# Optimization experiments

Hardware: AMD Instinct MI355X
Metric: run time of the kernel (lower is better)

Reference implementation:

```python
import jax, jax.numpy as jnp
import numpy as np

B, S, D, H = 4, 2048, 1024, 16
DK = D // H


def setup_inputs() -> dict:
    key = jax.random.key(0)
    ks = jax.random.split(key, 12)
    s = 1.0 / np.sqrt(D)
    return {
        "query": jax.random.normal(ks[0], (B, S, D), jnp.float32),
        "key": jax.random.normal(ks[1], (B, S, D), jnp.float32),
        "value": jax.random.normal(ks[2], (B, S, D), jnp.float32),
        "attention_mask": jax.random.randint(ks[3], (B, S, S), 0, 2, jnp.int32),
        "w_q": jax.random.uniform(ks[4], (D, D), jnp.float32, -s, s),
        "b_q": jax.random.uniform(ks[5], (D,), jnp.float32, -s, s),
        "w_k": jax.random.uniform(ks[6], (D, D), jnp.float32, -s, s),
        "b_k": jax.random.uniform(ks[7], (D,), jnp.float32, -s, s),
        "w_v": jax.random.uniform(ks[8], (D, D), jnp.float32, -s, s),
        "b_v": jax.random.uniform(ks[9], (D,), jnp.float32, -s, s),
        "w_o": jax.random.uniform(ks[10], (D, D), jnp.float32, -s, s),
        "b_o": jax.random.uniform(ks[11], (D,), jnp.float32, -s, s),
    }


def reference(query, key, value, attention_mask, w_q, b_q, w_k, b_k, w_v, b_v, w_o, b_o):
    # project and split heads: [B,S,D] -> [B,H,S,DK]
    def proj(x, w, b):
        y = jnp.einsum('bsd,ed->bse', x, w) + b  # torch Linear: x @ W.T + b
        return y.reshape(B, S, H, DK).transpose(0, 2, 1, 3)

    q = proj(query, w_q, b_q)
    k = proj(key, w_k, b_k)
    v = proj(value, w_v, b_v)

    scores = jnp.einsum('bhqd,bhkd->bhqk', q, k) / np.sqrt(DK).astype(np.float32)
    mask = attention_mask[:, None, :, :]  # broadcast over heads
    scores = jnp.where(mask == 0, jnp.float32(-1e9), scores)
    attn = jax.nn.softmax(scores, axis=-1)  # dropout is identity in eval
    out = jnp.einsum('bhqk,bhkd->bhqd', attn, v)
    out = out.transpose(0, 2, 1, 3).reshape(B, S, D)
    return jnp.einsum('bsd,ed->bse', out, w_o) + b_o
```

## Files before the change

kernel.cpp:

```cpp
#include <hip/hip_runtime.h>


#define B_ 4
#define S_ 2048
#define D_ 1024
#define H_ 16
#define DK_ 64
#define M_ (B_ * S_)

typedef __attribute__((ext_vector_type(4))) float f32x4;
typedef __attribute__((ext_vector_type(8))) short s16x8;
typedef __attribute__((ext_vector_type(8))) unsigned short u16x8;
typedef __attribute__((ext_vector_type(4))) unsigned short u16x4;

__device__ __forceinline__ unsigned short f2bf(float f) {
    union { float f; unsigned int u; } v; v.f = f;
    unsigned int u = v.u;
    return (unsigned short)((u + 0x7FFFu + ((u >> 16) & 1u)) >> 16);
}

__device__ __forceinline__ void gl2lds16(const unsigned short* g, unsigned short* l) {
    __builtin_amdgcn_global_load_lds((const __attribute__((address_space(1))) void*)g,
                                     (__attribute__((address_space(3))) void*)l, 16, 0, 0);
}

__global__ __launch_bounds__(256) void cvt_bf16(const float* __restrict__ x,
                                                unsigned short* __restrict__ y, int n) {
    int i = (blockIdx.x * 256 + threadIdx.x) * 8;
    if (i + 8 <= n) {
        float4 a = *(const float4*)(x + i);
        float4 b = *(const float4*)(x + i + 4);
        u16x8 r;
        r[0] = f2bf(a.x); r[1] = f2bf(a.y); r[2] = f2bf(a.z); r[3] = f2bf(a.w);
        r[4] = f2bf(b.x); r[5] = f2bf(b.y); r[6] = f2bf(b.z); r[7] = f2bf(b.w);
        *(u16x8*)(y + i) = r;
    }
}

__global__ __launch_bounds__(256) void pack_mask(const int* __restrict__ m,
                                                 unsigned long long* __restrict__ pm) {
    int t = blockIdx.x * 256 + threadIdx.x;
    unsigned long long bits = __ballot(m[t] != 0);
    if ((threadIdx.x & 63) == 0) pm[t >> 6] = bits;
}

template <int MODE>
__global__ __launch_bounds__(256) void gemm_bt(const unsigned short* __restrict__ A,
                                               const unsigned short* __restrict__ Bt,
                                               const float* __restrict__ bias,
                                               float scale, void* __restrict__ Y) {
    __shared__ __align__(16) unsigned short As[128 * 64];
    __shared__ __align__(16) unsigned short Bs[128 * 64];
    const int tid = threadIdx.x;
    const int wave = tid >> 6, lane = tid & 63, quad = lane >> 4, l16 = lane & 15;
    const int m0 = blockIdx.x * 128, n0 = blockIdx.y * 128;
    const int rw = (wave & 1) * 64, cw = (wave >> 1) * 64;
    const int sw = l16 & 7;

    const int srow = tid >> 3, scol = ((tid & 7) ^ (srow & 7)) * 8;
    const unsigned short* ga = A + (size_t)(m0 + srow) * 1024 + scol;
    const unsigned short* gb = Bt + (size_t)(n0 + srow) * 1024 + scol;

    f32x4 acc[4][4];
#pragma unroll
    for (int mi = 0; mi < 4; mi++)
#pragma unroll
        for (int ni = 0; ni < 4; ni++) acc[mi][ni] = (f32x4){0.f, 0.f, 0.f, 0.f};

    for (int k0 = 0; k0 < 1024; k0 += 64) {
#pragma unroll
        for (int r = 0; r < 4; r++) {
            gl2lds16(ga + (size_t)(r * 32) * 1024 + k0, &As[(r * 256 + tid) * 8]);
            gl2lds16(gb + (size_t)(r * 32) * 1024 + k0, &Bs[(r * 256 + tid) * 8]);
        }
        __syncthreads();
#pragma unroll
        for (int kki = 0; kki < 2; kki++) {
            const int xo = ((kki * 4 + quad) ^ sw) * 8;
            s16x8 af[4], bf[4];
#pragma unroll
            for (int mi = 0; mi < 4; mi++)
                af[mi] = *(const s16x8*)&As[(rw + mi * 16 + l16) * 64 + xo];
#pragma unroll
            for (int ni = 0; ni < 4; ni++)
                bf[ni] = *(const s16x8*)&Bs[(cw + ni * 16 + l16) * 64 + xo];
#pragma unroll
            for (int mi = 0; mi < 4; mi++)
#pragma unroll
                for (int ni = 0; ni < 4; ni++)
                    acc[mi][ni] = __builtin_amdgcn_mfma_f32_16x16x32_bf16(af[mi], bf[ni], acc[mi][ni], 0, 0, 0);
        }
        __syncthreads();
    }

    float bv[4];
#pragma unroll
    for (int ni = 0; ni < 4; ni++) bv[ni] = bias[n0 + cw + ni * 16 + l16];
#pragma unroll
    for (int mi = 0; mi < 4; mi++) {
        const int rb = m0 + rw + mi * 16 + quad * 4;
        const int b = rb >> 11, s0 = rb & 2047;
#pragma unroll
        for (int ni = 0; ni < 4; ni++) {
            const int col = n0 + cw + ni * 16 + l16;
            if (MODE == 3) {
#pragma unroll
                for (int i = 0; i < 4; i++)
                    ((float*)Y)[(size_t)(rb + i) * 1024 + col] = (acc[mi][ni][i] + bv[ni]) * scale;
            } else {
                const int h = col >> 6, dk = col & 63;
                if (MODE == 1) {
#pragma unroll
                    for (int i = 0; i < 4; i++)
                        ((unsigned short*)Y)[((size_t)(b * H_ + h) * S_ + s0 + i) * DK_ + dk] =
                            f2bf((acc[mi][ni][i] + bv[ni]) * scale);
                } else {
                    u16x4 pk;
#pragma unroll
                    for (int i = 0; i < 4; i++) pk[i] = f2bf((acc[mi][ni][i] + bv[ni]) * scale);
                    *(u16x4*)&((unsigned short*)Y)[((size_t)(b * H_ + h) * DK_ + dk) * S_ + s0] = pk;
                }
            }
        }
    }
}

__global__ __launch_bounds__(256) void attn_kernel(const unsigned short* __restrict__ Q,
                                                   const unsigned short* __restrict__ K,
                                                   const unsigned short* __restrict__ Vt,
                                                   const unsigned long long* __restrict__ pm,
                                                   unsigned short* __restrict__ ctx) {
    __shared__ __align__(16) unsigned short Ks[64 * 64];
    __shared__ __align__(16) unsigned short Vs[64 * 64];
    __shared__ __align__(16) unsigned short Ps[8 * 16 * 64];

    const int tid = threadIdx.x;
    const int wave = tid >> 6, lane = tid & 63, quad = lane >> 4, l16 = lane & 15;
    const int bh = blockIdx.y, b = bh >> 4, h = bh & 15;
    const int q0 = blockIdx.x * 128;
    const int qbase = q0 + wave * 32;
    const int sw = l16 & 7, q4 = quad * 4, qh = quad >> 1;

    const unsigned short* Kbase = K + (size_t)bh * S_ * DK_;
    const unsigned short* Vbase = Vt + (size_t)bh * DK_ * S_;

    s16x8 qf[2][2];
#pragma unroll
    for (int qb = 0; qb < 2; qb++) {
        const unsigned short* qr = Q + ((size_t)bh * S_ + qbase + qb * 16 + l16) * DK_ + quad * 8;
        qf[qb][0] = *(const s16x8*)qr;
        qf[qb][1] = *(const s16x8*)(qr + 32);
    }
    const unsigned long long* pmq[2];
#pragma unroll
    for (int qb = 0; qb < 2; qb++)
        pmq[qb] = pm + ((size_t)b * S_ + qbase + qb * 16 + l16) * 32;

    s16x8 ones;
#pragma unroll
    for (int j = 0; j < 8; j++) ones[j] = (short)0x3F80;

    f32x4 oacc[2][4], lacc[2];
#pragma unroll
    for (int qb = 0; qb < 2; qb++) {
        lacc[qb] = (f32x4){0.f, 0.f, 0.f, 0.f};
#pragma unroll
        for (int ct = 0; ct < 4; ct++) oacc[qb][ct] = (f32x4){0.f, 0.f, 0.f, 0.f};
    }

    const int sr = tid >> 3, sc = ((tid & 7) ^ (sr & 7)) * 8;

    for (int kt = 0; kt < S_ / 64; kt++) {
        const int k0 = kt * 64;
        gl2lds16(Kbase + (size_t)(k0 + sr) * DK_ + sc, &Ks[tid * 8]);
        gl2lds16(Kbase + (size_t)(k0 + 32 + sr) * DK_ + sc, &Ks[2048 + tid * 8]);
        gl2lds16(Vbase + (size_t)sr * S_ + k0 + sc, &Vs[tid * 8]);
        gl2lds16(Vbase + (size_t)(32 + sr) * S_ + k0 + sc, &Vs[2048 + tid * 8]);
        __syncthreads();

        f32x4 sacc[2][4];
#pragma unroll
        for (int qb = 0; qb < 2; qb++)
#pragma unroll
            for (int ct = 0; ct < 4; ct++) sacc[qb][ct] = (f32x4){0.f, 0.f, 0.f, 0.f};
#pragma unroll
        for (int kki = 0; kki < 2; kki++) {
            const int xo = ((kki * 4 + quad) ^ sw) * 8;
            s16x8 kf[4];
#pragma unroll
            for (int ct = 0; ct < 4; ct++)
                kf[ct] = *(const s16x8*)&Ks[(ct * 16 + l16) * 64 + xo];
#pragma unroll
            for (int qb = 0; qb < 2; qb++)
#pragma unroll
                for (int ct = 0; ct < 4; ct++)
                    sacc[qb][ct] = __builtin_amdgcn_mfma_f32_16x16x32_bf16(kf[ct], qf[qb][kki], sacc[qb][ct], 0, 0, 0);
        }

#pragma unroll
        for (int qb = 0; qb < 2; qb++) {
            unsigned short* pwq = &Ps[(wave * 2 + qb) * 1024];
            const uint2 mv = *(const uint2*)&pmq[qb][kt];
            const unsigned mqx = mv.x >> q4;
            const unsigned mqy = mv.y >> q4;
#pragma unroll
            for (int ct = 0; ct < 4; ct++) {
                const unsigned mq = (ct & 2) ? mqy : mqx;
                unsigned pu[4];
#pragma unroll
                for (int i = 0; i < 4; i++) {
                    const int pos = (ct & 1) * 16 + i;
                    const int mb = __builtin_amdgcn_sbfe(mq, pos, 1);
                    const float p = exp2f(sacc[qb][ct][i]);
                    pu[i] = __float_as_uint(p) & (unsigned)mb;
                }
                const int ch = ((2 * ct + qh) ^ sw) * 8;
#pragma unroll
                for (int t = 0; t < 2; t++) {
                    const unsigned pk = __builtin_amdgcn_perm(pu[2 * t + 1], pu[2 * t], 0x07060302u);
                    *(unsigned*)&pwq[l16 * 64 + ch + ((q4 + 2 * t) & 7)] = pk;
                }
            }
        }

#pragma unroll
        for (int kki = 0; kki < 2; kki++) {
            const int xo = ((kki * 4 + quad) ^ sw) * 8;
            s16x8 vf[4];
#pragma unroll
            for (int ct = 0; ct < 4; ct++)
                vf[ct] = *(const s16x8*)&Vs[(ct * 16 + l16) * 64 + xo];
#pragma unroll
            for (int qb = 0; qb < 2; qb++) {
                s16x8 pf = *(const s16x8*)&Ps[(wave * 2 + qb) * 1024 + l16 * 64 + xo];
#pragma unroll
                for (int ct = 0; ct < 4; ct++)
                    oacc[qb][ct] = __builtin_amdgcn_mfma_f32_16x16x32_bf16(pf, vf[ct], oacc[qb][ct], 0, 0, 0);
                lacc[qb] = __builtin_amdgcn_mfma_f32_16x16x32_bf16(pf, ones, lacc[qb], 0, 0, 0);
            }
        }
        __syncthreads();
    }

#pragma unroll
    for (int qb = 0; qb < 2; qb++) {
        f32x4 rl;
#pragma unroll
        for (int i = 0; i < 4; i++) rl[i] = 1.0f / lacc[qb][i];
#pragma unroll
        for (int ct = 0; ct < 4; ct++) {
            const int col = h * DK_ + ct * 16 + l16;
#pragma unroll
            for (int i = 0; i < 4; i++) {
                const int sg = qbase + qb * 16 + quad * 4 + i;
                ctx[((size_t)(b * S_ + sg)) * D_ + col] = f2bf(oacc[qb][ct][i] * rl[i]);
            }
        }
    }
}

extern "C" void kernel_launch(void* const* d_in, const int* in_sizes, int n_in,
                              void* d_out, int out_size, void* d_ws, size_t ws_size,
                              hipStream_t stream) {
    const float* query = (const float*)d_in[0];
    const float* key   = (const float*)d_in[1];
    const float* value = (const float*)d_in[2];
    const int*   mask  = (const int*)d_in[3];
    const float* w_q = (const float*)d_in[4];
    const float* b_q = (const float*)d_in[5];
    const float* w_k = (const float*)d_in[6];
    const float* b_k = (const float*)d_in[7];
    const float* w_v = (const float*)d_in[8];
    const float* b_v = (const float*)d_in[9];
    const float* w_o = (const float*)d_in[10];
    const float* b_o = (const float*)d_in[11];

    char* ws = (char*)d_ws;
    const size_t XSZ = (size_t)M_ * D_ * 2;
    const size_t WSZ = (size_t)D_ * D_ * 2;
    unsigned short* Xq  = (unsigned short*)(ws);
    unsigned short* Xk  = (unsigned short*)(ws + XSZ);
    unsigned short* Xv  = (unsigned short*)(ws + 2 * XSZ);
    unsigned short* Wq  = (unsigned short*)(ws + 3 * XSZ);
    unsigned short* Wk  = (unsigned short*)(ws + 3 * XSZ + WSZ);
    unsigned short* Wv  = (unsigned short*)(ws + 3 * XSZ + 2 * WSZ);
    unsigned short* Wo  = (unsigned short*)(ws + 3 * XSZ + 3 * WSZ);
    unsigned short* Qb  = (unsigned short*)(ws + 3 * XSZ + 4 * WSZ);
    unsigned short* Kb  = (unsigned short*)(ws + 4 * XSZ + 4 * WSZ);
    unsigned short* Vtb = (unsigned short*)(ws + 5 * XSZ + 4 * WSZ);
    unsigned short* ctx = (unsigned short*)(ws + 6 * XSZ + 4 * WSZ);
    unsigned long long* pm = (unsigned long long*)(ws);

    const int nTok = M_ * D_;
    const int nW = D_ * D_;
    hipLaunchKernelGGL(cvt_bf16, dim3(nTok / 2048), dim3(256), 0, stream, query, Xq, nTok);
    hipLaunchKernelGGL(cvt_bf16, dim3(nTok / 2048), dim3(256), 0, stream, key, Xk, nTok);
    hipLaunchKernelGGL(cvt_bf16, dim3(nTok / 2048), dim3(256), 0, stream, value, Xv, nTok);
    hipLaunchKernelGGL(cvt_bf16, dim3(nW / 2048), dim3(256), 0, stream, w_q, Wq, nW);
    hipLaunchKernelGGL(cvt_bf16, dim3(nW / 2048), dim3(256), 0, stream, w_k, Wk, nW);
    hipLaunchKernelGGL(cvt_bf16, dim3(nW / 2048), dim3(256), 0, stream, w_v, Wv, nW);
    hipLaunchKernelGGL(cvt_bf16, dim3(nW / 2048), dim3(256), 0, stream, w_o, Wo, nW);

    const float QSCALE = 0.125f * 1.44269504f;
    dim3 ggrid(M_ / 128, D_ / 128);
    hipLaunchKernelGGL(HIP_KERNEL_NAME(gemm_bt<1>), ggrid, dim3(256), 0, stream, Xq, Wq, b_q, QSCALE, (void*)Qb);
    hipLaunchKernelGGL(HIP_KERNEL_NAME(gemm_bt<1>), ggrid, dim3(256), 0, stream, Xk, Wk, b_k, 1.0f, (void*)Kb);
    hipLaunchKernelGGL(HIP_KERNEL_NAME(gemm_bt<2>), ggrid, dim3(256), 0, stream, Xv, Wv, b_v, 1.0f, (void*)Vtb);

    hipLaunchKernelGGL(pack_mask, dim3((B_ * S_ * S_) / 256), dim3(256), 0, stream, mask, pm);

    hipLaunchKernelGGL(attn_kernel, dim3(S_ / 128, B_ * H_), dim3(256), 0, stream,
                       Qb, Kb, Vtb, pm, ctx);

    hipLaunchKernelGGL(HIP_KERNEL_NAME(gemm_bt<3>), ggrid, dim3(256), 0, stream, ctx, Wo, b_o, 1.0f, d_out);
}
```

Measured before the change: 467.1 us.

## Load K/V fragments directly from global, pre-mask scores, batch conversion launches

The attention kernel no longer stages K and V tiles through shared memory with barriers. Each wave reads its MFMA fragments straight from global memory, relying on cache for reuse across waves. The mask is now packed inverted and applied by seeding the score accumulator with -inf for masked keys, so exp2 gives zero and the per-element AND after the exponential goes away. The seven fp32-to-bf16 conversion launches are merged into two launches. The trade is fewer syncs and no LDS staging against heavier, less-coalesced global loads and redundant K/V reads per wave.

```diff
diff --git a/kernel.cpp b/kernel.cpp
--- a/kernel.cpp
+++ b/kernel.cpp
@@ -24,8 +24,8 @@
                                      (__attribute__((address_space(3))) void*)l, 16, 0, 0);
 }
 
-__global__ __launch_bounds__(256) void cvt_bf16(const float* __restrict__ x,
-                                                unsigned short* __restrict__ y, int n) {
+__device__ __forceinline__ void cvt_body(const float* __restrict__ x,
+                                         unsigned short* __restrict__ y, int n) {
     int i = (blockIdx.x * 256 + threadIdx.x) * 8;
     if (i + 8 <= n) {
         float4 a = *(const float4*)(x + i);
@@ -37,10 +37,29 @@
     }
 }
 
+__global__ __launch_bounds__(256) void cvt_bf16x3(const float* __restrict__ x0, const float* __restrict__ x1,
+                                                  const float* __restrict__ x2, unsigned short* __restrict__ y0,
+                                                  unsigned short* __restrict__ y1, unsigned short* __restrict__ y2,
+                                                  int n) {
+    const float* x = blockIdx.y == 0 ? x0 : (blockIdx.y == 1 ? x1 : x2);
+    unsigned short* y = blockIdx.y == 0 ? y0 : (blockIdx.y == 1 ? y1 : y2);
+    cvt_body(x, y, n);
+}
+
+__global__ __launch_bounds__(256) void cvt_bf16x4(const float* __restrict__ x0, const float* __restrict__ x1,
+                                                  const float* __restrict__ x2, const float* __restrict__ x3,
+                                                  unsigned short* __restrict__ y0, unsigned short* __restrict__ y1,
+                                                  unsigned short* __restrict__ y2, unsigned short* __restrict__ y3,
+                                                  int n) {
+    const float* x = blockIdx.y == 0 ? x0 : (blockIdx.y == 1 ? x1 : (blockIdx.y == 2 ? x2 : x3));
+    unsigned short* y = blockIdx.y == 0 ? y0 : (blockIdx.y == 1 ? y1 : (blockIdx.y == 2 ? y2 : y3));
+    cvt_body(x, y, n);
+}
+
 __global__ __launch_bounds__(256) void pack_mask(const int* __restrict__ m,
                                                  unsigned long long* __restrict__ pm) {
     int t = blockIdx.x * 256 + threadIdx.x;
-    unsigned long long bits = __ballot(m[t] != 0);
+    unsigned long long bits = __ballot(m[t] == 0);
     if ((threadIdx.x & 63) == 0) pm[t >> 6] = bits;
 }
 
@@ -130,19 +149,16 @@
                                                    const unsigned short* __restrict__ Vt,
                                                    const unsigned long long* __restrict__ pm,
                                                    unsigned short* __restrict__ ctx) {
-    __shared__ __align__(16) unsigned short Ks[64 * 64];
-    __shared__ __align__(16) unsigned short Vs[64 * 64];
     __shared__ __align__(16) unsigned short Ps[8 * 16 * 64];
 
     const int tid = threadIdx.x;
     const int wave = tid >> 6, lane = tid & 63, quad = lane >> 4, l16 = lane & 15;
     const int bh = blockIdx.y, b = bh >> 4, h = bh & 15;
-    const int q0 = blockIdx.x * 128;
-    const int qbase = q0 + wave * 32;
+    const int qbase = blockIdx.x * 128 + wave * 32;
     const int sw = l16 & 7, q4 = quad * 4, qh = quad >> 1;
 
-    const unsigned short* Kbase = K + (size_t)bh * S_ * DK_;
-    const unsigned short* Vbase = Vt + (size_t)bh * DK_ * S_;
+    const unsigned short* Kfrag = K + ((size_t)bh * S_ + l16) * DK_ + quad * 8;
+    const unsigned short* Vfrag = Vt + ((size_t)bh * DK_ + l16) * S_ + quad * 8;
 
     s16x8 qf[2][2];
 #pragma unroll
@@ -168,28 +184,31 @@
         for (int ct = 0; ct < 4; ct++) oacc[qb][ct] = (f32x4){0.f, 0.f, 0.f, 0.f};
     }
 
-    const int sr = tid >> 3, sc = ((tid & 7) ^ (sr & 7)) * 8;
-
     for (int kt = 0; kt < S_ / 64; kt++) {
         const int k0 = kt * 64;
-        gl2lds16(Kbase + (size_t)(k0 + sr) * DK_ + sc, &Ks[tid * 8]);
-        gl2lds16(Kbase + (size_t)(k0 + 32 + sr) * DK_ + sc, &Ks[2048 + tid * 8]);
-        gl2lds16(Vbase + (size_t)sr * S_ + k0 + sc, &Vs[tid * 8]);
-        gl2lds16(Vbase + (size_t)(32 + sr) * S_ + k0 + sc, &Vs[2048 + tid * 8]);
-        __syncthreads();
 
         f32x4 sacc[2][4];
 #pragma unroll
-        for (int qb = 0; qb < 2; qb++)
-#pragma unroll
-            for (int ct = 0; ct < 4; ct++) sacc[qb][ct] = (f32x4){0.f, 0.f, 0.f, 0.f};
+        for (int qb = 0; qb < 2; qb++) {
+            const uint2 mv = *(const uint2*)&pmq[qb][kt];
+            const unsigned mqx = mv.x >> q4, mqy = mv.y >> q4;
+#pragma unroll
+            for (int ct = 0; ct < 4; ct++) {
+                const unsigned mq = (ct & 2) ? mqy : mqx;
+#pragma unroll
+                for (int i = 0; i < 4; i++) {
+                    const int mb = __builtin_amdgcn_sbfe(mq, (ct & 1) * 16 + i, 1);
+                    sacc[qb][ct][i] = __int_as_float(mb & (int)0xFF800000);
+                }
+            }
+        }
+
 #pragma unroll
         for (int kki = 0; kki < 2; kki++) {
-            const int xo = ((kki * 4 + quad) ^ sw) * 8;
             s16x8 kf[4];
 #pragma unroll
             for (int ct = 0; ct < 4; ct++)
-                kf[ct] = *(const s16x8*)&Ks[(ct * 16 + l16) * 64 + xo];
+                kf[ct] = *(const s16x8*)(Kfrag + (size_t)(k0 + ct * 16) * DK_ + kki * 32);
 #pragma unroll
             for (int qb = 0; qb < 2; qb++)
 #pragma unroll
@@ -200,20 +219,12 @@
 #pragma unroll
         for (int qb = 0; qb < 2; qb++) {
             unsigned short* pwq = &Ps[(wave * 2 + qb) * 1024];
-            const uint2 mv = *(const uint2*)&pmq[qb][kt];
-            const unsigned mqx = mv.x >> q4;
-            const unsigned mqy = mv.y >> q4;
 #pragma unroll
             for (int ct = 0; ct < 4; ct++) {
-                const unsigned mq = (ct & 2) ? mqy : mqx;
                 unsigned pu[4];
 #pragma unroll
-                for (int i = 0; i < 4; i++) {
-                    const int pos = (ct & 1) * 16 + i;
-                    const int mb = __builtin_amdgcn_sbfe(mq, pos, 1);
-                    const float p = exp2f(sacc[qb][ct][i]);
-                    pu[i] = __float_as_uint(p) & (unsigned)mb;
-                }
+                for (int i = 0; i < 4; i++)
+                    pu[i] = __float_as_uint(exp2f(sacc[qb][ct][i]));
                 const int ch = ((2 * ct + qh) ^ sw) * 8;
 #pragma unroll
                 for (int t = 0; t < 2; t++) {
@@ -229,7 +240,7 @@
             s16x8 vf[4];
 #pragma unroll
             for (int ct = 0; ct < 4; ct++)
-                vf[ct] = *(const s16x8*)&Vs[(ct * 16 + l16) * 64 + xo];
+                vf[ct] = *(const s16x8*)(Vfrag + (size_t)(ct * 16) * S_ + k0 + kki * 32);
 #pragma unroll
             for (int qb = 0; qb < 2; qb++) {
                 s16x8 pf = *(const s16x8*)&Ps[(wave * 2 + qb) * 1024 + l16 * 64 + xo];
@@ -239,7 +250,6 @@
                 lacc[qb] = __builtin_amdgcn_mfma_f32_16x16x32_bf16(pf, ones, lacc[qb], 0, 0, 0);
             }
         }
-        __syncthreads();
     }
 
 #pragma unroll
@@ -293,13 +303,10 @@
 
     const int nTok = M_ * D_;
     const int nW = D_ * D_;
-    hipLaunchKernelGGL(cvt_bf16, dim3(nTok / 2048), dim3(256), 0, stream, query, Xq, nTok);
-    hipLaunchKernelGGL(cvt_bf16, dim3(nTok / 2048), dim3(256), 0, stream, key, Xk, nTok);
-    hipLaunchKernelGGL(cvt_bf16, dim3(nTok / 2048), dim3(256), 0, stream, value, Xv, nTok);
-    hipLaunchKernelGGL(cvt_bf16, dim3(nW / 2048), dim3(256), 0, stream, w_q, Wq, nW);
-    hipLaunchKernelGGL(cvt_bf16, dim3(nW / 2048), dim3(256), 0, stream, w_k, Wk, nW);
-    hipLaunchKernelGGL(cvt_bf16, dim3(nW / 2048), dim3(256), 0, stream, w_v, Wv, nW);
-    hipLaunchKernelGGL(cvt_bf16, dim3(nW / 2048), dim3(256), 0, stream, w_o, Wo, nW);
+    hipLaunchKernelGGL(cvt_bf16x3, dim3(nTok / 2048, 3), dim3(256), 0, stream,
+                       query, key, value, Xq, Xk, Xv, nTok);
+    hipLaunchKernelGGL(cvt_bf16x4, dim3(nW / 2048, 4), dim3(256), 0, stream,
+                       w_q, w_k, w_v, w_o, Wq, Wk, Wv, Wo, nW);
 
     const float QSCALE = 0.125f * 1.44269504f;
     dim3 ggrid(M_ / 128, D_ / 128);
```

Result: slower. 568.1 us (+21.6%).
